# Kernel optimization log

Hardware: AMD Instinct MI355X
Metric: run time of the kernel (lower is better)

The kernel has to match this reference:

```python
import jax, jax.numpy as jnp
import numpy as np

NUM_HEADS = 12


def _rel_indices(H, W):
    # [N, N, 3] with channels (dx, dy, dx^2+dy^2), N = H*W
    indx = jnp.arange(W)[None, :] - jnp.arange(W)[:, None]          # [W, W]
    indx = jnp.tile(indx, (H, H))                                    # [N, N]
    indy = jnp.arange(H)[None, :] - jnp.arange(H)[:, None]          # [H, H]
    indy = jnp.repeat(jnp.repeat(indy, W, axis=0), W, axis=1)        # [N, N]
    indd = indx ** 2 + indy ** 2
    return jnp.stack([indx, indy, indd], axis=-1).astype(jnp.float32)


def setup_inputs() -> dict:
    key = jax.random.key(0)
    ks = jax.random.split(key, 8)
    B, N, C = 16, 576, 768
    std = 0.02
    return {
        "x": jax.random.normal(ks[0], (B, N, C), dtype=jnp.float32),
        "Wq": jax.random.normal(ks[1], (C, C), dtype=jnp.float32) * std,
        "Wk": jax.random.normal(ks[2], (C, C), dtype=jnp.float32) * std,
        "Wv": jax.random.normal(ks[3], (C, C), dtype=jnp.float32) * std,
        "Wproj": jax.random.normal(ks[4], (C, C), dtype=jnp.float32) * std,
        "bproj": jnp.zeros((C,), dtype=jnp.float32),
        "pos_w": jax.random.normal(ks[5], (3, NUM_HEADS), dtype=jnp.float32) * std,
        "pos_b": jnp.zeros((NUM_HEADS,), dtype=jnp.float32),
        "gating": jnp.ones((NUM_HEADS,), dtype=jnp.float32),
        "H": 24,
        "W": 24,
    }


def reference(x, Wq, Wk, Wv, Wproj, bproj, pos_w, pos_b, gating, H, W):
    B, N, C = x.shape
    h = gating.shape[0]
    d = C // h
    scale = d ** (-0.5)

    def heads(t):  # [B,N,C] -> [B,h,N,d]
        return t.reshape(B, N, h, d).transpose(0, 2, 1, 3)

    q = heads(x @ Wq)
    k = heads(x @ Wk)
    v = heads(x @ Wv)

    # content scores: [B,h,N,N]
    patch_score = jax.nn.softmax(jnp.einsum('bhnd,bhmd->bhnm', q, k) * scale, axis=-1)

    # positional scores: shared across batch, [h,N,N]
    rel = _rel_indices(H, W)                      # [N,N,3]
    pos_score = jnp.einsum('nmc,ch->hnm', rel, pos_w) + pos_b[:, None, None]
    pos_score = jax.nn.softmax(pos_score, axis=-1)

    gate = jax.nn.sigmoid(gating)[None, :, None, None]  # [1,h,1,1]
    attn = (1.0 - gate) * patch_score + gate * pos_score[None]
    attn = attn / jnp.sum(attn, axis=-1, keepdims=True)

    out = jnp.einsum('bhnm,bhmd->bhnd', attn, v)         # [B,h,N,d]
    out = out.transpose(0, 2, 1, 3).reshape(B, N, C)
    return out @ Wproj + bproj
```

## Files before the change

kernel.cpp:

```cpp
#include <hip/hip_runtime.h>
#include <math.h>

#define B_ 16
#define N_ 576
#define C_ 768
#define NH 12
#define D_ 64
#define STR 68

typedef unsigned short u16;
typedef __bf16 bf16x8 __attribute__((ext_vector_type(8)));
typedef float f32x4 __attribute__((ext_vector_type(4)));

__device__ __forceinline__ u16 f2bf(float f) {
    unsigned u = __builtin_bit_cast(unsigned, f);
    unsigned r = (u + 0x7FFFu + ((u >> 16) & 1u)) >> 16;
    return (u16)r;
}

__device__ __forceinline__ bf16x8 ldsF8u(const u16* p) {
    union { uint2 u[2]; bf16x8 v; } t;
    t.u[0] = *(const uint2*)p;
    t.u[1] = *(const uint2*)(p + 4);
    return t.v;
}
__device__ __forceinline__ bf16x8 ldsF8a(const u16* p) {
    union { uint4 u; bf16x8 v; } t;
    t.u = *(const uint4*)p;
    return t.v;
}

__device__ __forceinline__ void gload16(const u16* g, u16* l) {
    __builtin_amdgcn_global_load_lds(
        (const __attribute__((address_space(1))) void*)g,
        (__attribute__((address_space(3))) void*)l,
        16, 0, 0);
}

__global__ __launch_bounds__(256)
void conv_x_kernel(const float* __restrict__ x, u16* __restrict__ xb)
{
    int i = blockIdx.x * 256 + threadIdx.x;
    float4 v = ((const float4*)x)[i];
    u16 o[4] = {f2bf(v.x), f2bf(v.y), f2bf(v.z), f2bf(v.w)};
    *(uint2*)&xb[(size_t)i * 4] = *(const uint2*)o;
}

__global__ __launch_bounds__(256)
void transpose_w_kernel(const float* __restrict__ src, u16* __restrict__ dst)
{
    __shared__ float t[32][33];
    const int bx = blockIdx.x * 32, by = blockIdx.y * 32;
    const int tx = threadIdx.x & 31, ty = threadIdx.x >> 5;
#pragma unroll
    for (int i = 0; i < 32; i += 8)
        t[ty + i][tx] = src[(size_t)(by + ty + i) * C_ + bx + tx];
    __syncthreads();
#pragma unroll
    for (int i = 0; i < 32; i += 8)
        dst[(size_t)(bx + ty + i) * C_ + by + tx] = f2bf(t[tx][ty + i]);
}

__global__ __launch_bounds__(256)
void mfma_gemm(const u16* __restrict__ A,
               const u16* __restrict__ BT,
               const float* __restrict__ bias,
               float* __restrict__ out,
               u16* __restrict__ qb, u16* __restrict__ kb, u16* __restrict__ vtb,
               int mode)
{
    const int K = C_;
    __shared__ __align__(16) u16 As[128 * 32];
    __shared__ __align__(16) u16 Bs[128 * 32];
    const int tid = threadIdx.x;
    const int wave = tid >> 6, lane = tid & 63;
    const int quad = lane >> 4, l16 = lane & 15;
    const int wy = wave >> 1, wx = wave & 1;
    const int tm = blockIdx.y * 128, tn = blockIdx.x * 128;

    const int srow = lane >> 2;
    const int scol = (lane & 3) * 8;

    f32x4 acc[4][4];
#pragma unroll
    for (int i = 0; i < 4; ++i)
#pragma unroll
        for (int j = 0; j < 4; ++j)
            acc[i][j] = (f32x4){0.f, 0.f, 0.f, 0.f};

    for (int k0 = 0; k0 < K; k0 += 32) {
        __syncthreads();
#pragma unroll
        for (int p = 0; p < 2; ++p) {
            const int rg = p * 64 + wave * 16;
            gload16(A  + (size_t)(tm + rg + srow) * K + k0 + scol, &As[rg * 32]);
            gload16(BT + (size_t)(tn + rg + srow) * K + k0 + scol, &Bs[rg * 32]);
        }
        __syncthreads();

        bf16x8 aA[4], bB[4];
#pragma unroll
        for (int i = 0; i < 4; ++i)
            aA[i] = ldsF8a(&As[(wy * 64 + i * 16 + l16) * 32 + quad * 8]);
#pragma unroll
        for (int j = 0; j < 4; ++j)
            bB[j] = ldsF8a(&Bs[(wx * 64 + j * 16 + l16) * 32 + quad * 8]);
#pragma unroll
        for (int i = 0; i < 4; ++i)
#pragma unroll
            for (int j = 0; j < 4; ++j)
                acc[i][j] = __builtin_amdgcn_mfma_f32_16x16x32_bf16(aA[i], bB[j], acc[i][j], 0, 0, 0);
    }

    if (mode == 0) {
#pragma unroll
        for (int i = 0; i < 4; ++i) {
#pragma unroll
            for (int r = 0; r < 4; ++r) {
                const int m = tm + wy * 64 + i * 16 + quad * 4 + r;
#pragma unroll
                for (int j = 0; j < 4; ++j) {
                    const int c = tn + wx * 64 + j * 16 + l16;
                    out[(size_t)m * C_ + c] = acc[i][j][r] + bias[c];
                }
            }
        }
    } else {
        const int which = tn / C_;
        const int cb = tn % C_;
        const float scale = (which == 0) ? 0.125f : 1.0f;
#pragma unroll
        for (int i = 0; i < 4; ++i) {
#pragma unroll
            for (int r = 0; r < 4; ++r) {
                const int m = tm + wy * 64 + i * 16 + quad * 4 + r;
                const int b = m / N_, n = m % N_;
#pragma unroll
                for (int j = 0; j < 4; ++j) {
                    const int c = cb + wx * 64 + j * 16 + l16;
                    const int hh = c >> 6, dd = c & 63;
                    const u16 v = f2bf(acc[i][j][r] * scale);
                    if (which == 0)
                        qb[(((size_t)b * NH + hh) * N_ + n) * D_ + dd] = v;
                    else if (which == 1)
                        kb[(((size_t)b * NH + hh) * N_ + n) * D_ + dd] = v;
                    else
                        vtb[(((size_t)b * NH + hh) * D_ + dd) * N_ + n] = v;
                }
            }
        }
    }
}

__global__ __launch_bounds__(256)
void pos_softmax_kernel(const float* __restrict__ pos_w,
                        const float* __restrict__ pos_b,
                        const int* __restrict__ Hp,
                        const int* __restrict__ Wp,
                        u16* __restrict__ pos_out)
{
    const int n = blockIdx.x;
    const int hh = blockIdx.y;
    const int tid = threadIdx.x;
    __shared__ float srow[N_];
    __shared__ float wred[4];
    const int Ww = Wp[0];
    (void)Hp;
    const float w0 = pos_w[0 * NH + hh];
    const float w1 = pos_w[1 * NH + hh];
    const float w2 = pos_w[2 * NH + hh];
    const float bb = pos_b[hh];
    const int nx = n % Ww, ny = n / Ww;

    float lmax = -1e30f;
    for (int m = tid; m < N_; m += 256) {
        float dx = (float)((m % Ww) - nx);
        float dy = (float)((m / Ww) - ny);
        float sc = dx * w0 + dy * w1 + (dx * dx + dy * dy) * w2 + bb;
        srow[m] = sc;
        lmax = fmaxf(lmax, sc);
    }
#pragma unroll
    for (int off = 32; off; off >>= 1) lmax = fmaxf(lmax, __shfl_down(lmax, off, 64));
    if ((tid & 63) == 0) wred[tid >> 6] = lmax;
    __syncthreads();
    float M = fmaxf(fmaxf(wred[0], wred[1]), fmaxf(wred[2], wred[3]));
    __syncthreads();

    float lsum = 0.f;
    for (int m = tid; m < N_; m += 256) {
        float e = __expf(srow[m] - M);
        srow[m] = e;
        lsum += e;
    }
#pragma unroll
    for (int off = 32; off; off >>= 1) lsum += __shfl_down(lsum, off, 64);
    if ((tid & 63) == 0) wred[tid >> 6] = lsum;
    __syncthreads();
    float inv = 1.0f / (wred[0] + wred[1] + wred[2] + wred[3]);

    u16* op = pos_out + ((size_t)hh * N_ + n) * N_;
    for (int m = tid; m < N_; m += 256) op[m] = f2bf(srow[m] * inv);
}

__global__ __launch_bounds__(256)
void attn_kernel(const u16* __restrict__ q,
                 const u16* __restrict__ k,
                 const u16* __restrict__ vt,
                 const u16* __restrict__ pos,
                 const float* __restrict__ gating,
                 u16* __restrict__ ao)
{
    const int qt = blockIdx.x;
    const int bh = blockIdx.y;
    const int b = bh / NH, h = bh % NH;
    const int tid = threadIdx.x;
    const int wave = tid >> 6, lane = tid & 63;
    const int quad = lane >> 4, l16 = lane & 15;

    __shared__ u16 smem[4 * 64 * STR];
    u16* Kt = smem;
    u16* Vs = smem + 64 * STR;
    u16* Pp = smem + 2 * 64 * STR;
    u16* Pb = smem + 3 * 64 * STR;

    auto stage = [&](const u16* __restrict__ gsrc, size_t gs, u16* __restrict__ lds) {
#pragma unroll
        for (int p = 0; p < 2; ++p) {
            int idx = p * 256 + tid;
            int r = idx >> 3, c = (idx & 7) << 3;
            uint4 d = *(const uint4*)(gsrc + (size_t)r * gs + c);
            *(uint2*)&lds[r * STR + c]     = make_uint2(d.x, d.y);
            *(uint2*)&lds[r * STR + c + 4] = make_uint2(d.z, d.w);
        }
    };

    stage(q + ((size_t)bh * N_ + qt * 64) * D_, D_, Pb);
    __syncthreads();

    const int arow = wave * 16 + l16;
    bf16x8 aq0 = ldsF8u(&Pb[arow * STR + quad * 8]);
    bf16x8 aq1 = ldsF8u(&Pb[arow * STR + 32 + quad * 8]);

    f32x4 oc[4], op[4];
#pragma unroll
    for (int nt = 0; nt < 4; ++nt) {
        oc[nt] = (f32x4){0.f, 0.f, 0.f, 0.f};
        op[nt] = (f32x4){0.f, 0.f, 0.f, 0.f};
    }
    float lrun[4] = {0.f, 0.f, 0.f, 0.f};

    for (int mt = 0; mt < 9; ++mt) {
        const int m0 = mt * 64;
        __syncthreads();
        stage(k  + ((size_t)bh * N_ + m0) * D_, D_, Kt);
        stage(vt + ((size_t)bh * D_) * N_ + m0, N_, Vs);
        stage(pos + ((size_t)h * N_ + qt * 64) * N_ + m0, N_, Pp);
        __syncthreads();

        f32x4 s[4];
#pragma unroll
        for (int nt = 0; nt < 4; ++nt) {
            bf16x8 b0 = ldsF8u(&Kt[(nt * 16 + l16) * STR + quad * 8]);
            bf16x8 b1 = ldsF8u(&Kt[(nt * 16 + l16) * STR + 32 + quad * 8]);
            f32x4 z = (f32x4){0.f, 0.f, 0.f, 0.f};
            z = __builtin_amdgcn_mfma_f32_16x16x32_bf16(aq0, b0, z, 0, 0, 0);
            z = __builtin_amdgcn_mfma_f32_16x16x32_bf16(aq1, b1, z, 0, 0, 0);
            s[nt] = z;
        }

#pragma unroll
        for (int r = 0; r < 4; ++r) {
            const int prow = (wave * 16 + quad * 4 + r) * STR;
            float e0 = __expf(s[0][r]);
            float e1 = __expf(s[1][r]);
            float e2 = __expf(s[2][r]);
            float e3 = __expf(s[3][r]);
            Pb[prow +  0 + l16] = f2bf(e0);
            Pb[prow + 16 + l16] = f2bf(e1);
            Pb[prow + 32 + l16] = f2bf(e2);
            Pb[prow + 48 + l16] = f2bf(e3);
            lrun[r] += (e0 + e1) + (e2 + e3);
        }
        asm volatile("s_waitcnt lgkmcnt(0)" ::: "memory");

#pragma unroll
        for (int ks = 0; ks < 2; ++ks) {
            bf16x8 ap   = ldsF8u(&Pb[arow * STR + ks * 32 + quad * 8]);
            bf16x8 apos = ldsF8u(&Pp[arow * STR + ks * 32 + quad * 8]);
#pragma unroll
            for (int nt = 0; nt < 4; ++nt) {
                bf16x8 bv = ldsF8u(&Vs[(nt * 16 + l16) * STR + ks * 32 + quad * 8]);
                oc[nt] = __builtin_amdgcn_mfma_f32_16x16x32_bf16(ap,   bv, oc[nt], 0, 0, 0);
                op[nt] = __builtin_amdgcn_mfma_f32_16x16x32_bf16(apos, bv, op[nt], 0, 0, 0);
            }
        }
    }

#pragma unroll
    for (int r = 0; r < 4; ++r) {
        lrun[r] += __shfl_xor(lrun[r], 1, 64);
        lrun[r] += __shfl_xor(lrun[r], 2, 64);
        lrun[r] += __shfl_xor(lrun[r], 4, 64);
        lrun[r] += __shfl_xor(lrun[r], 8, 64);
    }

    const float g = 1.f / (1.f + __expf(-gating[h]));
#pragma unroll
    for (int r = 0; r < 4; ++r) {
        const float sc = (1.f - g) / lrun[r];
        const int row = qt * 64 + wave * 16 + quad * 4 + r;
#pragma unroll
        for (int nt = 0; nt < 4; ++nt) {
            ao[((size_t)b * N_ + row) * C_ + h * D_ + nt * 16 + l16] =
                f2bf(oc[nt][r] * sc + g * op[nt][r]);
        }
    }
}

extern "C" void kernel_launch(void* const* d_in, const int* in_sizes, int n_in,
                              void* d_out, int out_size, void* d_ws, size_t ws_size,
                              hipStream_t stream)
{
    const float* x      = (const float*)d_in[0];
    const float* Wq     = (const float*)d_in[1];
    const float* Wk     = (const float*)d_in[2];
    const float* Wv     = (const float*)d_in[3];
    const float* Wproj  = (const float*)d_in[4];
    const float* bproj  = (const float*)d_in[5];
    const float* pos_w  = (const float*)d_in[6];
    const float* pos_b  = (const float*)d_in[7];
    const float* gating = (const float*)d_in[8];
    const int*   Hp     = (const int*)d_in[9];
    const int*   Wp     = (const int*)d_in[10];
    float* out = (float*)d_out;

    const size_t xe  = (size_t)B_ * N_ * C_;
    const size_t we  = (size_t)C_ * C_;
    const size_t pe  = (size_t)NH * N_ * N_;
    u16* xb   = (u16*)d_ws;
    u16* wt   = xb + xe;
    u16* wtp  = wt + 3 * we;
    u16* qb   = wtp + we;
    u16* kb   = qb + xe;
    u16* vtb  = kb + xe;
    u16* posb = vtb + xe;
    u16* aob  = posb + pe;
    size_t need = (size_t)(5 * xe + 4 * we + pe) * sizeof(u16);
    if (ws_size < need) return;

    conv_x_kernel<<<dim3((unsigned)(xe / 1024)), 256, 0, stream>>>(x, xb);
    dim3 tgrid(24, 24);
    transpose_w_kernel<<<tgrid, 256, 0, stream>>>(Wq, wt);
    transpose_w_kernel<<<tgrid, 256, 0, stream>>>(Wk, wt + we);
    transpose_w_kernel<<<tgrid, 256, 0, stream>>>(Wv, wt + 2 * we);
    transpose_w_kernel<<<tgrid, 256, 0, stream>>>(Wproj, wtp);

    mfma_gemm<<<dim3(18, 72), 256, 0, stream>>>(xb, wt, nullptr, nullptr,
                                                qb, kb, vtb, 1);
    pos_softmax_kernel<<<dim3(N_, NH), 256, 0, stream>>>(pos_w, pos_b, Hp, Wp, posb);
    attn_kernel<<<dim3(9, B_ * NH), 256, 0, stream>>>(qb, kb, vtb, posb, gating, aob);
    mfma_gemm<<<dim3(6, 72), 256, 0, stream>>>(aob, wtp, bproj, out,
                                               nullptr, nullptr, nullptr, 0);
}
```

Measured before the change: 268.7 us.

## Write QKV row-major, transpose V separately, widen GEMM K-tile, prefetch attention tiles

The QKV GEMM now writes a plain row-major [B*N, 2304] bf16 buffer instead of scattering into per-head Q/K and a transposed V with strided stores. A separate small kernel transposes V through LDS. The GEMM K-step grows from 32 to 64 and uses an XOR-swizzled LDS layout to avoid bank conflicts. The attention kernel reads Q and K straight from the QKV buffer and register-prefetches the next K/V/pos tile while computing on the current one. In exchange it adds an extra kernel launch, an extra pass over V, and uses more registers and LDS.

```diff
diff --git a/kernel.cpp b/kernel.cpp
--- a/kernel.cpp
+++ b/kernel.cpp
@@ -7,6 +7,7 @@
 #define NH 12
 #define D_ 64
 #define STR 68
+#define QKV 2304
 
 typedef unsigned short u16;
 typedef __bf16 bf16x8 __attribute__((ext_vector_type(8)));
@@ -62,24 +63,52 @@
 }
 
 __global__ __launch_bounds__(256)
+void transpose_v_kernel(const u16* __restrict__ qkvb, u16* __restrict__ vtb)
+{
+    __shared__ u16 t[64 * 72];
+    const int n0 = blockIdx.x * 64;
+    const int bh = blockIdx.y;
+    const int b = bh / NH, h = bh % NH;
+    const int tid = threadIdx.x;
+    const u16* src = qkvb + ((size_t)b * N_ + n0) * QKV + 2 * C_ + h * D_;
+#pragma unroll
+    for (int p = 0; p < 2; ++p) {
+        int idx = p * 256 + tid;
+        int r = idx >> 3, c = (idx & 7) << 3;
+        *(uint4*)&t[r * 72 + c] = *(const uint4*)(src + (size_t)r * QKV + c);
+    }
+    __syncthreads();
+    u16* dst = vtb + (size_t)bh * D_ * N_ + n0;
+#pragma unroll
+    for (int p = 0; p < 2; ++p) {
+        int idx = p * 256 + tid;
+        int dd = idx >> 3, n8 = (idx & 7) << 3;
+        u16 o[8];
+#pragma unroll
+        for (int j = 0; j < 8; ++j) o[j] = t[(n8 + j) * 72 + dd];
+        *(uint4*)(dst + (size_t)dd * N_ + n8) = *(const uint4*)o;
+    }
+}
+
+__global__ __launch_bounds__(256)
 void mfma_gemm(const u16* __restrict__ A,
                const u16* __restrict__ BT,
                const float* __restrict__ bias,
                float* __restrict__ out,
-               u16* __restrict__ qb, u16* __restrict__ kb, u16* __restrict__ vtb,
-               int mode)
+               u16* __restrict__ outb,
+               int ldo, int mode)
 {
     const int K = C_;
-    __shared__ __align__(16) u16 As[128 * 32];
-    __shared__ __align__(16) u16 Bs[128 * 32];
+    __shared__ __align__(16) u16 As[128 * 64];
+    __shared__ __align__(16) u16 Bs[128 * 64];
     const int tid = threadIdx.x;
     const int wave = tid >> 6, lane = tid & 63;
     const int quad = lane >> 4, l16 = lane & 15;
     const int wy = wave >> 1, wx = wave & 1;
     const int tm = blockIdx.y * 128, tn = blockIdx.x * 128;
 
-    const int srow = lane >> 2;
-    const int scol = (lane & 3) * 8;
+    const int lr = lane >> 3;
+    const int sc = ((lane & 7) ^ lr) * 8;
 
     f32x4 acc[4][4];
 #pragma unroll
@@ -88,28 +117,35 @@
         for (int j = 0; j < 4; ++j)
             acc[i][j] = (f32x4){0.f, 0.f, 0.f, 0.f};
 
-    for (int k0 = 0; k0 < K; k0 += 32) {
+    for (int k0 = 0; k0 < K; k0 += 64) {
         __syncthreads();
 #pragma unroll
-        for (int p = 0; p < 2; ++p) {
-            const int rg = p * 64 + wave * 16;
-            gload16(A  + (size_t)(tm + rg + srow) * K + k0 + scol, &As[rg * 32]);
-            gload16(BT + (size_t)(tn + rg + srow) * K + k0 + scol, &Bs[rg * 32]);
+        for (int t = 0; t < 4; ++t) {
+            const int rg = wave * 32 + t * 8;
+            gload16(A  + (size_t)(tm + rg + lr) * K + k0 + sc, &As[rg * 64]);
+            gload16(BT + (size_t)(tn + rg + lr) * K + k0 + sc, &Bs[rg * 64]);
         }
         __syncthreads();
 
-        bf16x8 aA[4], bB[4];
-#pragma unroll
-        for (int i = 0; i < 4; ++i)
-            aA[i] = ldsF8a(&As[(wy * 64 + i * 16 + l16) * 32 + quad * 8]);
-#pragma unroll
-        for (int j = 0; j < 4; ++j)
-            bB[j] = ldsF8a(&Bs[(wx * 64 + j * 16 + l16) * 32 + quad * 8]);
-#pragma unroll
-        for (int i = 0; i < 4; ++i)
-#pragma unroll
-            for (int j = 0; j < 4; ++j)
-                acc[i][j] = __builtin_amdgcn_mfma_f32_16x16x32_bf16(aA[i], bB[j], acc[i][j], 0, 0, 0);
+#pragma unroll
+        for (int kh = 0; kh < 2; ++kh) {
+            bf16x8 aA[4], bB[4];
+#pragma unroll
+            for (int i = 0; i < 4; ++i) {
+                const int s = (kh * 4 + quad) ^ (l16 & 7);
+                aA[i] = ldsF8a(&As[(wy * 64 + i * 16 + l16) * 64 + s * 8]);
+            }
+#pragma unroll
+            for (int j = 0; j < 4; ++j) {
+                const int s = (kh * 4 + quad) ^ (l16 & 7);
+                bB[j] = ldsF8a(&Bs[(wx * 64 + j * 16 + l16) * 64 + s * 8]);
+            }
+#pragma unroll
+            for (int i = 0; i < 4; ++i)
+#pragma unroll
+                for (int j = 0; j < 4; ++j)
+                    acc[i][j] = __builtin_amdgcn_mfma_f32_16x16x32_bf16(aA[i], bB[j], acc[i][j], 0, 0, 0);
+        }
     }
 
     if (mode == 0) {
@@ -121,31 +157,21 @@
 #pragma unroll
                 for (int j = 0; j < 4; ++j) {
                     const int c = tn + wx * 64 + j * 16 + l16;
-                    out[(size_t)m * C_ + c] = acc[i][j][r] + bias[c];
+                    out[(size_t)m * ldo + c] = acc[i][j][r] + bias[c];
                 }
             }
         }
     } else {
-        const int which = tn / C_;
-        const int cb = tn % C_;
-        const float scale = (which == 0) ? 0.125f : 1.0f;
+        const float scale = (tn < C_) ? 0.125f : 1.0f;
 #pragma unroll
         for (int i = 0; i < 4; ++i) {
 #pragma unroll
             for (int r = 0; r < 4; ++r) {
                 const int m = tm + wy * 64 + i * 16 + quad * 4 + r;
-                const int b = m / N_, n = m % N_;
 #pragma unroll
                 for (int j = 0; j < 4; ++j) {
-                    const int c = cb + wx * 64 + j * 16 + l16;
-                    const int hh = c >> 6, dd = c & 63;
-                    const u16 v = f2bf(acc[i][j][r] * scale);
-                    if (which == 0)
-                        qb[(((size_t)b * NH + hh) * N_ + n) * D_ + dd] = v;
-                    else if (which == 1)
-                        kb[(((size_t)b * NH + hh) * N_ + n) * D_ + dd] = v;
-                    else
-                        vtb[(((size_t)b * NH + hh) * D_ + dd) * N_ + n] = v;
+                    const int c = tn + wx * 64 + j * 16 + l16;
+                    outb[(size_t)m * ldo + c] = f2bf(acc[i][j][r] * scale);
                 }
             }
         }
@@ -204,8 +230,7 @@
 }
 
 __global__ __launch_bounds__(256)
-void attn_kernel(const u16* __restrict__ q,
-                 const u16* __restrict__ k,
+void attn_kernel(const u16* __restrict__ qkvb,
                  const u16* __restrict__ vt,
                  const u16* __restrict__ pos,
                  const float* __restrict__ gating,
@@ -224,24 +249,52 @@
     u16* Pp = smem + 2 * 64 * STR;
     u16* Pb = smem + 3 * 64 * STR;
 
-    auto stage = [&](const u16* __restrict__ gsrc, size_t gs, u16* __restrict__ lds) {
-#pragma unroll
-        for (int p = 0; p < 2; ++p) {
-            int idx = p * 256 + tid;
-            int r = idx >> 3, c = (idx & 7) << 3;
-            uint4 d = *(const uint4*)(gsrc + (size_t)r * gs + c);
-            *(uint2*)&lds[r * STR + c]     = make_uint2(d.x, d.y);
-            *(uint2*)&lds[r * STR + c + 4] = make_uint2(d.z, d.w);
-        }
-    };
-
-    stage(q + ((size_t)bh * N_ + qt * 64) * D_, D_, Pb);
+    const u16* qptr  = qkvb + ((size_t)b * N_ + qt * 64) * QKV + h * D_;
+    const u16* kbase = qkvb + (size_t)b * N_ * QKV + C_ + h * D_;
+    const u16* vbase = vt + (size_t)bh * D_ * N_;
+    const u16* pbase = pos + ((size_t)h * N_ + qt * 64) * N_;
+
+    const int sr = tid >> 3;
+    const int scol = (tid & 7) << 3;
+
+#pragma unroll
+    for (int p = 0; p < 2; ++p) {
+        int r = p * 32 + sr;
+        uint4 d = *(const uint4*)(qptr + (size_t)r * QKV + scol);
+        *(uint2*)&Pb[r * STR + scol]     = make_uint2(d.x, d.y);
+        *(uint2*)&Pb[r * STR + scol + 4] = make_uint2(d.z, d.w);
+    }
     __syncthreads();
 
     const int arow = wave * 16 + l16;
     bf16x8 aq0 = ldsF8u(&Pb[arow * STR + quad * 8]);
     bf16x8 aq1 = ldsF8u(&Pb[arow * STR + 32 + quad * 8]);
 
+    uint4 rk[2], rv[2], rp[2];
+    auto loadT = [&](int m0) {
+#pragma unroll
+        for (int p = 0; p < 2; ++p) {
+            int r = p * 32 + sr;
+            rk[p] = *(const uint4*)(kbase + (size_t)(m0 + r) * QKV + scol);
+            rv[p] = *(const uint4*)(vbase + (size_t)r * N_ + m0 + scol);
+            rp[p] = *(const uint4*)(pbase + (size_t)r * N_ + m0 + scol);
+        }
+    };
+    auto writeT = [&]() {
+#pragma unroll
+        for (int p = 0; p < 2; ++p) {
+            int r = p * 32 + sr;
+            *(uint2*)&Kt[r * STR + scol]     = make_uint2(rk[p].x, rk[p].y);
+            *(uint2*)&Kt[r * STR + scol + 4] = make_uint2(rk[p].z, rk[p].w);
+            *(uint2*)&Vs[r * STR + scol]     = make_uint2(rv[p].x, rv[p].y);
+            *(uint2*)&Vs[r * STR + scol + 4] = make_uint2(rv[p].z, rv[p].w);
+            *(uint2*)&Pp[r * STR + scol]     = make_uint2(rp[p].x, rp[p].y);
+            *(uint2*)&Pp[r * STR + scol + 4] = make_uint2(rp[p].z, rp[p].w);
+        }
+    };
+
+    loadT(0);
+
     f32x4 oc[4], op[4];
 #pragma unroll
     for (int nt = 0; nt < 4; ++nt) {
@@ -251,12 +304,10 @@
     float lrun[4] = {0.f, 0.f, 0.f, 0.f};
 
     for (int mt = 0; mt < 9; ++mt) {
-        const int m0 = mt * 64;
         __syncthreads();
-        stage(k  + ((size_t)bh * N_ + m0) * D_, D_, Kt);
-        stage(vt + ((size_t)bh * D_) * N_ + m0, N_, Vs);
-        stage(pos + ((size_t)h * N_ + qt * 64) * N_ + m0, N_, Pp);
+        writeT();
         __syncthreads();
+        if (mt < 8) loadT((mt + 1) * 64);
 
         f32x4 s[4];
 #pragma unroll
@@ -335,18 +386,18 @@
     const int*   Wp     = (const int*)d_in[10];
     float* out = (float*)d_out;
 
-    const size_t xe  = (size_t)B_ * N_ * C_;
-    const size_t we  = (size_t)C_ * C_;
-    const size_t pe  = (size_t)NH * N_ * N_;
+    const size_t xe = (size_t)B_ * N_ * C_;
+    const size_t we = (size_t)C_ * C_;
+    const size_t qe = (size_t)B_ * N_ * QKV;
+    const size_t pe = (size_t)NH * N_ * N_;
     u16* xb   = (u16*)d_ws;
     u16* wt   = xb + xe;
     u16* wtp  = wt + 3 * we;
-    u16* qb   = wtp + we;
-    u16* kb   = qb + xe;
-    u16* vtb  = kb + xe;
+    u16* qkvb = wtp + we;
+    u16* vtb  = qkvb + qe;
     u16* posb = vtb + xe;
     u16* aob  = posb + pe;
-    size_t need = (size_t)(5 * xe + 4 * we + pe) * sizeof(u16);
+    size_t need = (size_t)(3 * xe + 4 * we + qe + pe) * sizeof(u16);
     if (ws_size < need) return;
 
     conv_x_kernel<<<dim3((unsigned)(xe / 1024)), 256, 0, stream>>>(x, xb);
@@ -357,9 +408,10 @@
     transpose_w_kernel<<<tgrid, 256, 0, stream>>>(Wproj, wtp);
 
     mfma_gemm<<<dim3(18, 72), 256, 0, stream>>>(xb, wt, nullptr, nullptr,
-                                                qb, kb, vtb, 1);
+                                                qkvb, QKV, 1);
+    transpose_v_kernel<<<dim3(9, B_ * NH), 256, 0, stream>>>(qkvb, vtb);
     pos_softmax_kernel<<<dim3(N_, NH), 256, 0, stream>>>(pos_w, pos_b, Hp, Wp, posb);
-    attn_kernel<<<dim3(9, B_ * NH), 256, 0, stream>>>(qb, kb, vtb, posb, gating, aob);
+    attn_kernel<<<dim3(9, B_ * NH), 256, 0, stream>>>(qkvb, vtb, posb, gating, aob);
     mfma_gemm<<<dim3(6, 72), 256, 0, stream>>>(aob, wtp, bproj, out,
-                                               nullptr, nullptr, nullptr, 0);
-}
+                                               nullptr, C_, 0);
+}
```

New measurement: 246.9 us. 1.09x faster.
